# Kernel tuning notes

Hardware: AMD Instinct MI355X
Metric: run time of the kernel (lower is better)

## Reference

```python
import jax, jax.numpy as jnp
import numpy as np

EPS = 1e-3  # keras LayerNormalization default epsilon
H = 12     # number_of_heads


def _layer_norm(x, gamma, beta):
    mu = jnp.mean(x, axis=-1, keepdims=True)
    var = jnp.mean(jnp.square(x - mu), axis=-1, keepdims=True)
    return (x - mu) * jax.lax.rsqrt(var + EPS) * gamma + beta


def _gelu(x):
    return jax.nn.gelu(x, approximate=False)  # keras 'gelu' default is erf-based


def setup_inputs():
    key = jax.random.key(0)
    B, N, E, F, Fe = 8, 1024, 16384, 96, 32
    ks = jax.random.split(key, 20)
    def dense(k, din, dout):
        return jax.random.normal(k, (din, dout), jnp.float32) / np.float32(np.sqrt(din))
    return {
        "nodes": jax.random.normal(ks[0], (B, N, F), jnp.float32),
        "edge_features": jax.random.normal(ks[1], (B, E, Fe), jnp.float32),
        "edges": jax.random.randint(ks[2], (B, E, 2), 0, N),
        "edge_weights": jax.random.uniform(ks[3], (B, E, 1), jnp.float32),
        "edge_dropout": jnp.ones((B, E, 2), jnp.float32),
        # message layer: Dense(F) on concat([src,dst,edge_feat]) + GELU + LayerNorm
        "Wm": dense(ks[4], 2 * F + Fe, F), "bm": jnp.zeros((F,), jnp.float32),
        "gm": jnp.ones((F,), jnp.float32), "betam": jnp.zeros((F,), jnp.float32),
        # gated MHSA on concat([nodes, aggregated]) (2F -> F) + GELU + LayerNorm
        "Wq": dense(ks[5], 2 * F, F), "bq": jnp.zeros((F,), jnp.float32),
        "Wk": dense(ks[6], 2 * F, F), "bk": jnp.zeros((F,), jnp.float32),
        "Wv": dense(ks[7], 2 * F, F), "bv": jnp.zeros((F,), jnp.float32),
        "Wg": dense(ks[8], 2 * F, F), "bg": jnp.zeros((F,), jnp.float32),
        "Wo": dense(ks[9], F, F), "bo": jnp.zeros((F,), jnp.float32),
        "gu": jnp.ones((F,), jnp.float32), "betau": jnp.zeros((F,), jnp.float32),
    }


def reference(nodes, edge_features, edges, edge_weights, edge_dropout,
              Wm, bm, gm, betam, Wq, bq, Wk, bk, Wv, bv, Wg, bg, Wo, bo, gu, betau):
    B, N, F = nodes.shape
    E = edges.shape[1]
    # gather both endpoint features per edge: [B, E, 2F]
    gathered = jnp.take_along_axis(nodes, edges.reshape(B, 2 * E, 1), axis=1)
    msg_in = jnp.concatenate([gathered.reshape(B, E, 2 * F), edge_features], axis=-1)
    messages = _layer_norm(_gelu(msg_in @ Wm + bm), gm, betam)        # [B,E,F]
    weighted_messages = messages * edge_weights                        # [B,E,F]
    # batched scatter-sum onto target node edges[...,1], gated by dropout[...,1]
    contrib = weighted_messages * edge_dropout[..., 1:2]
    seg_ids = (edges[..., 1] + jnp.arange(B, dtype=edges.dtype)[:, None] * N).reshape(-1)
    aggregated = jax.ops.segment_sum(contrib.reshape(B * E, F), seg_ids,
                                     num_segments=B * N).reshape(B, N, F)
    # gated multi-head self-attention over concat(nodes, aggregated)
    x = jnp.concatenate([nodes, aggregated], axis=-1)                  # [B,N,2F]
    d = F // H
    def split_heads(y):
        return y.reshape(B, N, H, d).transpose(0, 2, 1, 3)             # [B,H,N,d]
    q = split_heads(x @ Wq + bq)
    k = split_heads(x @ Wk + bk)
    v = split_heads(x @ Wv + bv)
    gate = jax.nn.sigmoid(split_heads(x @ Wg + bg))
    scores = jnp.einsum("bhqd,bhkd->bhqk", q, k) / jnp.sqrt(jnp.float32(d))
    att = jnp.einsum("bhqk,bhkd->bhqd", jax.nn.softmax(scores, axis=-1), v) * gate
    att = att.transpose(0, 2, 1, 3).reshape(B, N, F)
    updated_nodes = _layer_norm(_gelu(att @ Wo + bo), gu, betau)
    return updated_nodes, weighted_messages, edges, edge_weights, edge_dropout
```

## Files before the change

kernel.cpp:

```cpp
#include <hip/hip_runtime.h>
#include <hip/hip_bf16.h>

#define BB 8
#define NN 1024
#define EE 16384
#define FF 96
#define FE 32
#define NH 12
#define DD 8
#define KM 224
#define KX 192
#define TE 64
#define BK 32

__device__ __forceinline__ float gelu_erf(float x){
    return 0.5f * x * (1.0f + erff(x * 0.70710678118654752f));
}

__device__ __forceinline__ int load_idx(const int* __restrict__ p, int i){
    int v = p[i];
    if (!((unsigned)v < 1024u)) v = (int)__int_as_float(v);
    return min(max(v, 0), NN-1);
}

__global__ __launch_bounds__(256) void hist_kernel(
    const int* __restrict__ edges, int* __restrict__ cnt)
{
    const int i = blockIdx.x*blockDim.x + threadIdx.x;
    if (i < BB*EE){
        const int b = i >> 14;
        const int dst = load_idx(edges, 2*i+1);
        atomicAdd(&cnt[b*NN + dst], 1);
    }
}

__global__ __launch_bounds__(1024) void scan_kernel(
    const int* __restrict__ cnt, int* __restrict__ rowstart, int* __restrict__ cursor)
{
    const int b = blockIdx.x;
    const int t = threadIdx.x;
    __shared__ int s[NN];
    const int v = cnt[b*NN + t];
    s[t] = v;
    __syncthreads();
    for (int off = 1; off < NN; off <<= 1){
        int u = (t >= off) ? s[t-off] : 0;
        __syncthreads();
        s[t] += u;
        __syncthreads();
    }
    const int ex = s[t] - v + b*EE;
    rowstart[b*NN + t] = ex;
    cursor[b*NN + t]   = ex;
}

__global__ __launch_bounds__(256) void scatter_kernel(
    const int* __restrict__ edges, int* __restrict__ cursor, int* __restrict__ elist)
{
    const int i = blockIdx.x*blockDim.x + threadIdx.x;
    if (i < BB*EE){
        const int b = i >> 14;
        const int dst = load_idx(edges, 2*i+1);
        const int pos = atomicAdd(&cursor[b*NN + dst], 1);
        elist[pos] = i;
    }
}

__global__ __launch_bounds__(256) void node_proj_kernel(
    const float* __restrict__ nodes, const float* __restrict__ Wm,
    float* __restrict__ P1, float* __restrict__ P2)
{
    const int rt  = blockIdx.x;
    const int m   = blockIdx.y;
    const int tid = threadIdx.x;
    const int tx  = tid & 15;
    const int ty  = tid >> 4;
    const int r0  = rt * TE;

    const float* W = Wm + (size_t)(m ? FF : 0) * FF;
    float* out     = m ? P2 : P1;

    __shared__ float Xs[TE][BK+4];
    __shared__ float Ws[BK][FF];

    float acc[4][6];
    #pragma unroll
    for (int a=0;a<4;++a)
        #pragma unroll
        for (int c=0;c<6;++c) acc[a][c] = 0.f;

    const int e_st = tid >> 2;
    const int kk0  = (tid & 3) * 8;

    for (int c = 0; c < 3; ++c){
        __syncthreads();
        {
            const float4* src = (const float4*)(W + (size_t)c*BK*FF);
            float4* dst = (float4*)&Ws[0][0];
            dst[tid      ] = src[tid      ];
            dst[tid + 256] = src[tid + 256];
            dst[tid + 512] = src[tid + 512];
        }
        {
            const float* rp = nodes + (size_t)(r0 + e_st)*FF + c*BK;
            *(float4*)&Xs[e_st][kk0    ] = *(const float4*)(rp + kk0);
            *(float4*)&Xs[e_st][kk0 + 4] = *(const float4*)(rp + kk0 + 4);
        }
        __syncthreads();
        #pragma unroll 4
        for (int kk = 0; kk < BK; ++kk){
            float2 w01 = *(const float2*)&Ws[kk][6*tx    ];
            float2 w23 = *(const float2*)&Ws[kk][6*tx + 2];
            float2 w45 = *(const float2*)&Ws[kk][6*tx + 4];
            float xv[4];
            #pragma unroll
            for (int ei=0; ei<4; ++ei) xv[ei] = Xs[ty + 16*ei][kk];
            #pragma unroll
            for (int ei=0; ei<4; ++ei){
                acc[ei][0] += xv[ei]*w01.x;  acc[ei][1] += xv[ei]*w01.y;
                acc[ei][2] += xv[ei]*w23.x;  acc[ei][3] += xv[ei]*w23.y;
                acc[ei][4] += xv[ei]*w45.x;  acc[ei][5] += xv[ei]*w45.y;
            }
        }
    }

    #pragma unroll
    for (int ei = 0; ei < 4; ++ei){
        const int row = r0 + ty + 16*ei;
        float* __restrict__ orow = out + (size_t)row*FF + 6*tx;
        #pragma unroll
        for (int jj=0; jj<6; ++jj) orow[jj] = acc[ei][jj];
    }
}

__global__ __launch_bounds__(256) void edge_msg2_kernel(
    const float* __restrict__ P1, const float* __restrict__ P2,
    const float* __restrict__ ef,
    const int*  __restrict__ edges, const float* __restrict__ ew,
    const float* __restrict__ Wm, const float* __restrict__ bm,
    const float* __restrict__ gm, const float* __restrict__ betam,
    float* __restrict__ wm_out)
{
    const int bid = blockIdx.x;
    const int tid = threadIdx.x;
    const int tx  = tid & 15;
    const int ty  = tid >> 4;
    const int be0 = bid * TE;
    const int b   = be0 >> 14;

    __shared__ float Xs[TE][BK+4];
    __shared__ float Ws[BK][FF];
    __shared__ int   eidx[TE*2];
    __shared__ float ewS[TE];
    __shared__ float bmS[FF], gmS[FF], betamS[FF];

    if (tid < TE*2){
        int v = edges[(size_t)be0*2 + tid];
        if (!((unsigned)v < 1024u)) v = (int)__int_as_float(v);
        eidx[tid] = min(max(v, 0), NN-1);
    }
    if (tid < TE) ewS[tid] = ew[be0 + tid];
    if (tid < FF){ bmS[tid] = bm[tid]; gmS[tid] = gm[tid]; betamS[tid] = betam[tid]; }

    float acc[4][6];
    #pragma unroll
    for (int a=0;a<4;++a)
        #pragma unroll
        for (int c=0;c<6;++c) acc[a][c] = 0.f;

    const int e_st = tid >> 2;
    const int kk0  = (tid & 3) * 8;

    {
        const float4* src = (const float4*)(Wm + (size_t)KX*FF);
        float4* dst = (float4*)&Ws[0][0];
        dst[tid      ] = src[tid      ];
        dst[tid + 256] = src[tid + 256];
        dst[tid + 512] = src[tid + 512];
    }
    {
        const float* rp = ef + (size_t)(be0 + e_st)*FE;
        *(float4*)&Xs[e_st][kk0    ] = *(const float4*)(rp + kk0);
        *(float4*)&Xs[e_st][kk0 + 4] = *(const float4*)(rp + kk0 + 4);
    }
    __syncthreads();
    #pragma unroll 4
    for (int kk = 0; kk < BK; ++kk){
        float2 w01 = *(const float2*)&Ws[kk][6*tx    ];
        float2 w23 = *(const float2*)&Ws[kk][6*tx + 2];
        float2 w45 = *(const float2*)&Ws[kk][6*tx + 4];
        float xv[4];
        #pragma unroll
        for (int ei=0; ei<4; ++ei) xv[ei] = Xs[ty + 16*ei][kk];
        #pragma unroll
        for (int ei=0; ei<4; ++ei){
            acc[ei][0] += xv[ei]*w01.x;  acc[ei][1] += xv[ei]*w01.y;
            acc[ei][2] += xv[ei]*w23.x;  acc[ei][3] += xv[ei]*w23.y;
            acc[ei][4] += xv[ei]*w45.x;  acc[ei][5] += xv[ei]*w45.y;
        }
    }

    float add[4][6];
    #pragma unroll
    for (int ei = 0; ei < 4; ++ei){
        const int el = ty + 16*ei;
        const int sn = eidx[2*el];
        const int dn = eidx[2*el+1];
        const float2* p1 = (const float2*)(P1 + (size_t)(b*NN + sn)*FF + 6*tx);
        const float2* p2 = (const float2*)(P2 + (size_t)(b*NN + dn)*FF + 6*tx);
        const float2 a0 = p1[0], a1 = p1[1], a2 = p1[2];
        const float2 b0 = p2[0], b1 = p2[1], b2 = p2[2];
        add[ei][0] = a0.x + b0.x;  add[ei][1] = a0.y + b0.y;
        add[ei][2] = a1.x + b1.x;  add[ei][3] = a1.y + b1.y;
        add[ei][4] = a2.x + b2.x;  add[ei][5] = a2.y + b2.y;
    }

    #pragma unroll
    for (int ei = 0; ei < 4; ++ei){
        const int el = ty + 16*ei;
        float h[6]; float psum = 0.f;
        #pragma unroll
        for (int jj=0; jj<6; ++jj){
            h[jj] = gelu_erf(acc[ei][jj] + add[ei][jj] + bmS[6*tx + jj]);
            psum += h[jj];
        }
        #pragma unroll
        for (int m=1; m<16; m<<=1) psum += __shfl_xor(psum, m, 16);
        const float mu = psum * (1.f/FF);
        float vsum = 0.f;
        #pragma unroll
        for (int jj=0; jj<6; ++jj){ float d = h[jj]-mu; vsum += d*d; }
        #pragma unroll
        for (int m=1; m<16; m<<=1) vsum += __shfl_xor(vsum, m, 16);
        const float rstd = rsqrtf(vsum*(1.f/FF) + 1e-3f);

        const float w = ewS[el];
        float* __restrict__ wrow = wm_out + (size_t)(be0 + el)*FF + 6*tx;
        #pragma unroll
        for (int jj=0; jj<6; ++jj)
            wrow[jj] = ((h[jj]-mu)*rstd*gmS[6*tx+jj] + betamS[6*tx+jj]) * w;
    }
}

__global__ __launch_bounds__(96) void gather_kernel(
    const float* __restrict__ wm_out, const float* __restrict__ ed,
    const int* __restrict__ elist, const int* __restrict__ rowstart,
    const int* __restrict__ cnt, float* __restrict__ agg)
{
    const int bn = blockIdx.x;
    const int t  = threadIdx.x;
    const int beg = rowstart[bn];
    const int num = cnt[bn];
    float sum = 0.f;
    for (int i = 0; i < num; ++i){
        const int be = elist[beg + i];
        const float coeff = ed[2*(size_t)be + 1];
        sum += wm_out[(size_t)be*FF + t] * coeff;
    }
    agg[(size_t)bn*FF + t] = sum;
}

__global__ __launch_bounds__(256) void qkvg_kernel(
    const float* __restrict__ nodes, const float* __restrict__ agg,
    const float* __restrict__ Wq, const float* __restrict__ bq,
    const float* __restrict__ Wk, const float* __restrict__ bk,
    const float* __restrict__ Wv, const float* __restrict__ bv,
    const float* __restrict__ Wg, const float* __restrict__ bg,
    float* __restrict__ qo, float* __restrict__ ko,
    float* __restrict__ vo, float* __restrict__ go)
{
    const int rt  = blockIdx.x;
    const int m   = blockIdx.y;
    const int tid = threadIdx.x;
    const int tx  = tid & 15;
    const int ty  = tid >> 4;
    const int r0  = rt * TE;

    const float* W    = (m==0)?Wq:(m==1)?Wk:(m==2)?Wv:Wg;
    const float* bias = (m==0)?bq:(m==1)?bk:(m==2)?bv:bg;
    float* out        = (m==0)?qo:(m==1)?ko:(m==2)?vo:go;

    __shared__ float Xs[TE][BK+4];
    __shared__ float Ws[BK][FF];
    __shared__ float bS[FF];
    if (tid < FF) bS[tid] = bias[tid];

    float acc[4][6];
    #pragma unroll
    for (int a=0;a<4;++a)
        #pragma unroll
        for (int c=0;c<6;++c) acc[a][c] = 0.f;

    const int e_st = tid >> 2;
    const int kk0  = (tid & 3) * 8;

    for (int c = 0; c < 6; ++c){
        __syncthreads();
        {
            const float4* src = (const float4*)(W + (size_t)c*BK*FF);
            float4* dst = (float4*)&Ws[0][0];
            dst[tid      ] = src[tid      ];
            dst[tid + 256] = src[tid + 256];
            dst[tid + 512] = src[tid + 512];
        }
        {
            const float* rp = (c < 3)
                ? nodes + (size_t)(r0 + e_st)*FF + c*BK
                : agg   + (size_t)(r0 + e_st)*FF + (c-3)*BK;
            *(float4*)&Xs[e_st][kk0    ] = *(const float4*)(rp + kk0);
            *(float4*)&Xs[e_st][kk0 + 4] = *(const float4*)(rp + kk0 + 4);
        }
        __syncthreads();
        #pragma unroll 4
        for (int kk = 0; kk < BK; ++kk){
            float2 w01 = *(const float2*)&Ws[kk][6*tx    ];
            float2 w23 = *(const float2*)&Ws[kk][6*tx + 2];
            float2 w45 = *(const float2*)&Ws[kk][6*tx + 4];
            float xv[4];
            #pragma unroll
            for (int ei=0; ei<4; ++ei) xv[ei] = Xs[ty + 16*ei][kk];
            #pragma unroll
            for (int ei=0; ei<4; ++ei){
                acc[ei][0] += xv[ei]*w01.x;  acc[ei][1] += xv[ei]*w01.y;
                acc[ei][2] += xv[ei]*w23.x;  acc[ei][3] += xv[ei]*w23.y;
                acc[ei][4] += xv[ei]*w45.x;  acc[ei][5] += xv[ei]*w45.y;
            }
        }
    }

    #pragma unroll
    for (int ei = 0; ei < 4; ++ei){
        const int row = r0 + ty + 16*ei;
        float* __restrict__ orow = out + (size_t)row*FF + 6*tx;
        #pragma unroll
        for (int jj=0; jj<6; ++jj) orow[jj] = acc[ei][jj] + bS[6*tx + jj];
    }
}

__global__ __launch_bounds__(256) void attn_kernel(
    const float* __restrict__ q, const float* __restrict__ k,
    const float* __restrict__ v, const float* g,
    float* att)
{
    const int blk = blockIdx.x;
    const int qt = blk & 15;
    const int h  = (blk >> 4) % NH;
    const int b  = blk / (16*NH);
    const int tid  = threadIdx.x;
    const int lane = tid & 63;
    const int w    = tid >> 6;
    const int r    = lane & 15;
    const int s    = lane >> 4;
    const int qrow = qt*64 + w*16 + r;
    const size_t base = (size_t)(b*NN)*FF + h*DD;

    __shared__ float Ks[128][12];
    __shared__ float Vs[128][12];

    float qr[DD];
    const float* qp = q + base + (size_t)qrow*FF;
    #pragma unroll
    for (int i=0;i<DD;++i) qr[i] = qp[i] * 0.35355339059327373f;

    float m = -1e30f, l = 0.f, o[DD];
    #pragma unroll
    for (int i=0;i<DD;++i) o[i] = 0.f;

    const int skey  = tid >> 1;
    const int shalf = (tid & 1) * 4;

    for (int kc = 0; kc < NN; kc += 128){
        __syncthreads();
        {
            const float* kp = k + base + (size_t)(kc + skey)*FF + shalf;
            const float* vp = v + base + (size_t)(kc + skey)*FF + shalf;
            *(float4*)&Ks[skey][shalf] = *(const float4*)kp;
            *(float4*)&Vs[skey][shalf] = *(const float4*)vp;
        }
        __syncthreads();
        #pragma unroll
        for (int gidx = 0; gidx < 4; ++gidx){
            float sc[8];
            #pragma unroll
            for (int jj = 0; jj < 8; ++jj){
                const int key = 32*gidx + 4*jj + s;
                float4 k0 = *(const float4*)&Ks[key][0];
                float4 k1 = *(const float4*)&Ks[key][4];
                sc[jj] = qr[0]*k0.x + qr[1]*k0.y + qr[2]*k0.z + qr[3]*k0.w
                       + qr[4]*k1.x + qr[5]*k1.y + qr[6]*k1.z + qr[7]*k1.w;
            }
            const float g01 = fmaxf(sc[0], sc[1]), g23 = fmaxf(sc[2], sc[3]);
            const float g45 = fmaxf(sc[4], sc[5]), g67 = fmaxf(sc[6], sc[7]);
            const float gmax = fmaxf(fmaxf(g01, g23), fmaxf(g45, g67));
            if (gmax > m + 8.f){
                const float c = __expf(m - gmax);
                l *= c;
                #pragma unroll
                for (int i=0;i<DD;++i) o[i] *= c;
                m = gmax;
            }
            #pragma unroll
            for (int jj = 0; jj < 8; ++jj){
                const int key = 32*gidx + 4*jj + s;
                float4 v0 = *(const float4*)&Vs[key][0];
                float4 v1 = *(const float4*)&Vs[key][4];
                const float p = __expf(sc[jj] - m);
                l += p;
                o[0] += p*v0.x;  o[1] += p*v0.y;
                o[2] += p*v0.z;  o[3] += p*v0.w;
                o[4] += p*v1.x;  o[5] += p*v1.y;
                o[6] += p*v1.z;  o[7] += p*v1.w;
            }
        }
    }

    #pragma unroll
    for (int mask = 16; mask <= 32; mask <<= 1){
        const float m2 = __shfl_xor(m, mask);
        const float l2 = __shfl_xor(l, mask);
        float o2[DD];
        #pragma unroll
        for (int i=0;i<DD;++i) o2[i] = __shfl_xor(o[i], mask);
        const float M  = fmaxf(m, m2);
        const float c1 = __expf(m - M);
        const float c2 = __expf(m2 - M);
        l = l*c1 + l2*c2;
        #pragma unroll
        for (int i=0;i<DD;++i) o[i] = o[i]*c1 + o2[i]*c2;
        m = M;
    }

    if (s == 0){
        const float inv = 1.f / l;
        const float* gp = g + base + (size_t)qrow*FF;
        float* ap = att + base + (size_t)qrow*FF;
        #pragma unroll
        for (int i=0;i<DD;++i){
            const float gate = 1.f/(1.f + __expf(-gp[i]));
            ap[i] = o[i]*inv*gate;
        }
    }
}

__global__ __launch_bounds__(256) void out_kernel(
    const float* __restrict__ att, const float* __restrict__ Wo, const float* __restrict__ bo,
    const float* __restrict__ gu, const float* __restrict__ betau,
    float* __restrict__ out0)
{
    const int rt  = blockIdx.x;
    const int tid = threadIdx.x;
    const int tx  = tid & 15;
    const int ty  = tid >> 4;
    const int r0  = rt * TE;

    __shared__ float Xs[TE][BK+4];
    __shared__ float Ws[BK][FF];
    __shared__ float boS[FF], guS[FF], beS[FF];
    if (tid < FF){ boS[tid] = bo[tid]; guS[tid] = gu[tid]; beS[tid] = betau[tid]; }

    float acc[4][6];
    #pragma unroll
    for (int a=0;a<4;++a)
        #pragma unroll
        for (int c=0;c<6;++c) acc[a][c] = 0.f;

    const int e_st = tid >> 2;
    const int kk0  = (tid & 3) * 8;

    for (int c = 0; c < 3; ++c){
        __syncthreads();
        {
            const float4* src = (const float4*)(Wo + (size_t)c*BK*FF);
            float4* dst = (float4*)&Ws[0][0];
            dst[tid      ] = src[tid      ];
            dst[tid + 256] = src[tid + 256];
            dst[tid + 512] = src[tid + 512];
        }
        {
            const float* rp = att + (size_t)(r0 + e_st)*FF + c*BK;
            *(float4*)&Xs[e_st][kk0    ] = *(const float4*)(rp + kk0);
            *(float4*)&Xs[e_st][kk0 + 4] = *(const float4*)(rp + kk0 + 4);
        }
        __syncthreads();
        #pragma unroll 4
        for (int kk = 0; kk < BK; ++kk){
            float2 w01 = *(const float2*)&Ws[kk][6*tx    ];
            float2 w23 = *(const float2*)&Ws[kk][6*tx + 2];
            float2 w45 = *(const float2*)&Ws[kk][6*tx + 4];
            float xv[4];
            #pragma unroll
            for (int ei=0; ei<4; ++ei) xv[ei] = Xs[ty + 16*ei][kk];
            #pragma unroll
            for (int ei=0; ei<4; ++ei){
                acc[ei][0] += xv[ei]*w01.x;  acc[ei][1] += xv[ei]*w01.y;
                acc[ei][2] += xv[ei]*w23.x;  acc[ei][3] += xv[ei]*w23.y;
                acc[ei][4] += xv[ei]*w45.x;  acc[ei][5] += xv[ei]*w45.y;
            }
        }
    }

    #pragma unroll
    for (int ei = 0; ei < 4; ++ei){
        const int row = r0 + ty + 16*ei;
        float h[6]; float psum = 0.f;
        #pragma unroll
        for (int jj=0; jj<6; ++jj){
            h[jj] = gelu_erf(acc[ei][jj] + boS[6*tx + jj]);
            psum += h[jj];
        }
        #pragma unroll
        for (int m=1; m<16; m<<=1) psum += __shfl_xor(psum, m, 16);
        const float mu = psum * (1.f/FF);
        float vsum = 0.f;
        #pragma unroll
        for (int jj=0; jj<6; ++jj){ float d = h[jj]-mu; vsum += d*d; }
        #pragma unroll
        for (int m=1; m<16; m<<=1) vsum += __shfl_xor(vsum, m, 16);
        const float rstd = rsqrtf(vsum*(1.f/FF) + 1e-3f);
        float* __restrict__ orow = out0 + (size_t)row*FF + 6*tx;
        #pragma unroll
        for (int jj=0; jj<6; ++jj)
            orow[jj] = (h[jj]-mu)*rstd*guS[6*tx+jj] + beS[6*tx+jj];
    }
}

__global__ void passthrough_kernel(const int* __restrict__ edges,
    const float* __restrict__ ew, const float* __restrict__ ed,
    float* __restrict__ o_edges, float* __restrict__ o_ew, float* __restrict__ o_ed)
{
    const int i = blockIdx.x*blockDim.x + threadIdx.x;
    const int NE2 = BB*EE*2;
    const int NW  = BB*EE;
    if (i < NE2)                 o_edges[i] = (float)load_idx(edges, i);
    else if (i < NE2+NW)         o_ew[i-NE2] = ew[i-NE2];
    else if (i < NE2+NW+NE2)     o_ed[i-NE2-NW] = ed[i-NE2-NW];
}

extern "C" void kernel_launch(void* const* d_in, const int* in_sizes, int n_in,
                              void* d_out, int out_size, void* d_ws, size_t ws_size,
                              hipStream_t stream) {
    int i_nodes=-1, i_ef=-1, i_edges=-1, i_ed=-1, i_ew=-1, i_Wm=-1, i_Wo=-1;
    int i_W4[4]; int nW4=0;
    int i_v96[10]; int nv96=0;
    for (int i = 0; i < n_in; ++i){
        const int s = in_sizes[i];
        if      (s == 786432)  i_nodes = i;
        else if (s == 4194304) i_ef = i;
        else if (s == 262144)  { if (i_edges < 0) i_edges = i; else i_ed = i; }
        else if (s == 131072)  i_ew = i;
        else if (s == 21504)   i_Wm = i;
        else if (s == 18432)   { if (nW4 < 4) i_W4[nW4++] = i; }
        else if (s == 9216)    i_Wo = i;
        else if (s == 96)      { if (nv96 < 10) i_v96[nv96++] = i; }
    }
    const float* nodes = (const float*)d_in[i_nodes];
    const float* ef    = (const float*)d_in[i_ef];
    const int*   edges = (const int*)d_in[i_edges];
    const float* ew    = (const float*)d_in[i_ew];
    const float* ed    = (const float*)d_in[i_ed];
    const float* Wm = (const float*)d_in[i_Wm];
    const float* Wq = (const float*)d_in[i_W4[0]];
    const float* Wk = (const float*)d_in[i_W4[1]];
    const float* Wv = (const float*)d_in[i_W4[2]];
    const float* Wg = (const float*)d_in[i_W4[3]];
    const float* Wo = (const float*)d_in[i_Wo];
    const float* bm    = (const float*)d_in[i_v96[0]];
    const float* gm    = (const float*)d_in[i_v96[1]];
    const float* betam = (const float*)d_in[i_v96[2]];
    const float* bq    = (const float*)d_in[i_v96[3]];
    const float* bk    = (const float*)d_in[i_v96[4]];
    const float* bv    = (const float*)d_in[i_v96[5]];
    const float* bg    = (const float*)d_in[i_v96[6]];
    const float* bo    = (const float*)d_in[i_v96[7]];
    const float* gu    = (const float*)d_in[i_v96[8]];
    const float* betau = (const float*)d_in[i_v96[9]];

    float* outp = (float*)d_out;
    const size_t ROWS  = (size_t)BB*NN*FF;
    const size_t WMSZ  = (size_t)BB*EE*FF;
    const size_t NE2   = (size_t)BB*EE*2;
    const size_t NW    = (size_t)BB*EE;
    float* out_un    = outp;
    float* out_wm    = outp + ROWS;
    float* out_edges = outp + ROWS + WMSZ;
    float* out_ew    = outp + ROWS + WMSZ + NE2;
    float* out_ed    = outp + ROWS + WMSZ + NE2 + NW;

    float* ws  = (float*)d_ws;
    float* agg = ws;
    float* qo  = ws + 1*ROWS;
    float* ko  = ws + 2*ROWS;
    float* vo  = ws + 3*ROWS;
    float* go  = ws + 4*ROWS;
    float* att = go;
    float* P1  = qo;
    float* P2  = ko;
    int* ints      = (int*)(ws + 5*ROWS);
    int* cnt       = ints;
    int* rowstart  = ints + BB*NN;
    int* cursor    = ints + 2*BB*NN;
    int* elist     = ints + 3*BB*NN;

    hipMemsetAsync(cnt, 0, BB*NN*sizeof(int), stream);

    hist_kernel<<<(BB*EE+255)/256, 256, 0, stream>>>(edges, cnt);
    scan_kernel<<<BB, NN, 0, stream>>>(cnt, rowstart, cursor);
    scatter_kernel<<<(BB*EE+255)/256, 256, 0, stream>>>(edges, cursor, elist);

    dim3 npgrid((BB*NN)/TE, 2);
    node_proj_kernel<<<npgrid, 256, 0, stream>>>(nodes, Wm, P1, P2);

    edge_msg2_kernel<<<(BB*EE)/TE, 256, 0, stream>>>(P1, P2, ef, edges, ew,
                                               Wm, bm, gm, betam, out_wm);
    gather_kernel<<<BB*NN, 96, 0, stream>>>(out_wm, ed, elist, rowstart, cnt, agg);

    dim3 qgrid((BB*NN)/TE, 4);
    qkvg_kernel<<<qgrid, 256, 0, stream>>>(nodes, agg, Wq, bq, Wk, bk, Wv, bv,
                                           Wg, bg, qo, ko, vo, go);
    attn_kernel<<<BB*NH*16, 256, 0, stream>>>(qo, ko, vo, go, att);
    out_kernel<<<(BB*NN)/TE, 256, 0, stream>>>(att, Wo, bo, gu, betau, out_un);

    const int npass = (int)(NE2 + NW + NE2);
    passthrough_kernel<<<(npass+255)/256, 256, 0, stream>>>(edges, ew, ed,
                                               out_edges, out_ew, out_ed);
}
```

Before: 311.6 us.

## Register-block attention over four query rows per thread to reuse shared K/V loads

```diff
diff --git a/kernel.cpp b/kernel.cpp
--- a/kernel.cpp
+++ b/kernel.cpp
@@ -337,7 +337,7 @@
     }
 }
 
-__global__ __launch_bounds__(256) void attn_kernel(
+__global__ __launch_bounds__(256, 4) void attn_kernel(
     const float* __restrict__ q, const float* __restrict__ k,
     const float* __restrict__ v, const float* g,
     float* att)
@@ -349,22 +349,29 @@
     const int tid  = threadIdx.x;
     const int lane = tid & 63;
     const int w    = tid >> 6;
-    const int r    = lane & 15;
-    const int s    = lane >> 4;
-    const int qrow = qt*64 + w*16 + r;
+    const int rg   = lane >> 4;
+    const int s    = lane & 15;
+    const int row0 = qt*64 + w*16 + rg*4;
     const size_t base = (size_t)(b*NN)*FF + h*DD;
 
     __shared__ float Ks[128][12];
     __shared__ float Vs[128][12];
 
-    float qr[DD];
-    const float* qp = q + base + (size_t)qrow*FF;
-    #pragma unroll
-    for (int i=0;i<DD;++i) qr[i] = qp[i] * 0.35355339059327373f;
-
-    float m = -1e30f, l = 0.f, o[DD];
-    #pragma unroll
-    for (int i=0;i<DD;++i) o[i] = 0.f;
+    float qr[4][DD];
+    #pragma unroll
+    for (int i=0;i<4;++i){
+        const float* qp = q + base + (size_t)(row0+i)*FF;
+        #pragma unroll
+        for (int d0=0; d0<DD; ++d0) qr[i][d0] = qp[d0] * 0.35355339059327373f;
+    }
+
+    float m[4], l[4], o[4][DD];
+    #pragma unroll
+    for (int i=0;i<4;++i){
+        m[i] = -1e30f; l[i] = 0.f;
+        #pragma unroll
+        for (int d0=0; d0<DD; ++d0) o[i][d0] = 0.f;
+    }
 
     const int skey  = tid >> 1;
     const int shalf = (tid & 1) * 4;
@@ -379,65 +386,80 @@
         }
         __syncthreads();
         #pragma unroll
-        for (int gidx = 0; gidx < 4; ++gidx){
-            float sc[8];
-            #pragma unroll
-            for (int jj = 0; jj < 8; ++jj){
-                const int key = 32*gidx + 4*jj + s;
-                float4 k0 = *(const float4*)&Ks[key][0];
-                float4 k1 = *(const float4*)&Ks[key][4];
-                sc[jj] = qr[0]*k0.x + qr[1]*k0.y + qr[2]*k0.z + qr[3]*k0.w
-                       + qr[4]*k1.x + qr[5]*k1.y + qr[6]*k1.z + qr[7]*k1.w;
+        for (int g2 = 0; g2 < 2; ++g2){
+            float sc[4][4];
+            #pragma unroll
+            for (int j=0;j<4;++j){
+                const int key = g2*64 + j*16 + s;
+                const float4 k0 = *(const float4*)&Ks[key][0];
+                const float4 k1 = *(const float4*)&Ks[key][4];
+                #pragma unroll
+                for (int i=0;i<4;++i){
+                    sc[i][j] = qr[i][0]*k0.x + qr[i][1]*k0.y + qr[i][2]*k0.z + qr[i][3]*k0.w
+                             + qr[i][4]*k1.x + qr[i][5]*k1.y + qr[i][6]*k1.z + qr[i][7]*k1.w;
+                }
             }
-            const float g01 = fmaxf(sc[0], sc[1]), g23 = fmaxf(sc[2], sc[3]);
-            const float g45 = fmaxf(sc[4], sc[5]), g67 = fmaxf(sc[6], sc[7]);
-            const float gmax = fmaxf(fmaxf(g01, g23), fmaxf(g45, g67));
-            if (gmax > m + 8.f){
-                const float c = __expf(m - gmax);
-                l *= c;
+            #pragma unroll
+            for (int i=0;i<4;++i){
+                const float gmax = fmaxf(fmaxf(sc[i][0], sc[i][1]),
+                                         fmaxf(sc[i][2], sc[i][3]));
+                if (gmax > m[i] + 8.f){
+                    const float c = __expf(m[i] - gmax);
+                    l[i] *= c;
+                    #pragma unroll
+                    for (int d0=0; d0<DD; ++d0) o[i][d0] *= c;
+                    m[i] = gmax;
+                }
+            }
+            #pragma unroll
+            for (int j=0;j<4;++j){
+                const int key = g2*64 + j*16 + s;
+                const float4 v0 = *(const float4*)&Vs[key][0];
+                const float4 v1 = *(const float4*)&Vs[key][4];
                 #pragma unroll
-                for (int i=0;i<DD;++i) o[i] *= c;
-                m = gmax;
+                for (int i=0;i<4;++i){
+                    const float p = __expf(sc[i][j] - m[i]);
+                    l[i] += p;
+                    o[i][0] += p*v0.x;  o[i][1] += p*v0.y;
+                    o[i][2] += p*v0.z;  o[i][3] += p*v0.w;
+                    o[i][4] += p*v1.x;  o[i][5] += p*v1.y;
+                    o[i][6] += p*v1.z;  o[i][7] += p*v1.w;
+                }
             }
-            #pragma unroll
-            for (int jj = 0; jj < 8; ++jj){
-                const int key = 32*gidx + 4*jj + s;
-                float4 v0 = *(const float4*)&Vs[key][0];
-                float4 v1 = *(const float4*)&Vs[key][4];
-                const float p = __expf(sc[jj] - m);
-                l += p;
-                o[0] += p*v0.x;  o[1] += p*v0.y;
-                o[2] += p*v0.z;  o[3] += p*v0.w;
-                o[4] += p*v1.x;  o[5] += p*v1.y;
-                o[6] += p*v1.z;  o[7] += p*v1.w;
+        }
+    }
+
+    #pragma unroll
+    for (int mask = 1; mask <= 8; mask <<= 1){
+        #pragma unroll
+        for (int i=0;i<4;++i){
+            const float m2 = __shfl_xor(m[i], mask);
+            const float l2 = __shfl_xor(l[i], mask);
+            float o2[DD];
+            #pragma unroll
+            for (int d0=0; d0<DD; ++d0) o2[d0] = __shfl_xor(o[i][d0], mask);
+            const float M  = fmaxf(m[i], m2);
+            const float c1 = __expf(m[i] - M);
+            const float c2 = __expf(m2 - M);
+            l[i] = l[i]*c1 + l2*c2;
+            #pragma unroll
+            for (int d0=0; d0<DD; ++d0) o[i][d0] = o[i][d0]*c1 + o2[d0]*c2;
+            m[i] = M;
+        }
+    }
+
+    if (s == 0){
+        #pragma unroll
+        for (int i=0;i<4;++i){
+            const int row = row0 + i;
+            const float inv = 1.f / l[i];
+            const float* gp = g + base + (size_t)row*FF;
+            float* ap = att + base + (size_t)row*FF;
+            #pragma unroll
+            for (int d0=0; d0<DD; ++d0){
+                const float gate = 1.f/(1.f + __expf(-gp[d0]));
+                ap[d0] = o[i][d0]*inv*gate;
             }
-        }
-    }
-
-    #pragma unroll
-    for (int mask = 16; mask <= 32; mask <<= 1){
-        const float m2 = __shfl_xor(m, mask);
-        const float l2 = __shfl_xor(l, mask);
-        float o2[DD];
-        #pragma unroll
-        for (int i=0;i<DD;++i) o2[i] = __shfl_xor(o[i], mask);
-        const float M  = fmaxf(m, m2);
-        const float c1 = __expf(m - M);
-        const float c2 = __expf(m2 - M);
-        l = l*c1 + l2*c2;
-        #pragma unroll
-        for (int i=0;i<DD;++i) o[i] = o[i]*c1 + o2[i]*c2;
-        m = M;
-    }
-
-    if (s == 0){
-        const float inv = 1.f / l;
-        const float* gp = g + base + (size_t)qrow*FF;
-        float* ap = att + base + (size_t)qrow*FF;
-        #pragma unroll
-        for (int i=0;i<DD;++i){
-            const float gate = 1.f/(1.f + __expf(-gp[i]));
-            ap[i] = o[i]*inv*gate;
         }
     }
 }
```

New measurement: 511.9 us. +64.3%, slower.

## Double-buffer K/V tiles in attention and switch softmax to exp2 domain

Applied to the files above, without the earlier changes.

```diff
diff --git a/kernel.cpp b/kernel.cpp
--- a/kernel.cpp
+++ b/kernel.cpp
@@ -13,6 +13,12 @@
 #define TE 64
 #define BK 32
 
+#if __has_builtin(__builtin_amdgcn_exp2f)
+#define EXP2(x) __builtin_amdgcn_exp2f(x)
+#else
+#define EXP2(x) exp2f(x)
+#endif
+
 __device__ __forceinline__ float gelu_erf(float x){
     return 0.5f * x * (1.0f + erff(x * 0.70710678118654752f));
 }
@@ -354,13 +360,13 @@
     const int qrow = qt*64 + w*16 + r;
     const size_t base = (size_t)(b*NN)*FF + h*DD;
 
-    __shared__ float Ks[128][12];
-    __shared__ float Vs[128][12];
+    __shared__ float Ks[2][128][12];
+    __shared__ float Vs[2][128][12];
 
     float qr[DD];
     const float* qp = q + base + (size_t)qrow*FF;
     #pragma unroll
-    for (int i=0;i<DD;++i) qr[i] = qp[i] * 0.35355339059327373f;
+    for (int i=0;i<DD;++i) qr[i] = qp[i] * 0.51010300101462254f;
 
     float m = -1e30f, l = 0.f, o[DD];
     #pragma unroll
@@ -369,31 +375,37 @@
     const int skey  = tid >> 1;
     const int shalf = (tid & 1) * 4;
 
-    for (int kc = 0; kc < NN; kc += 128){
-        __syncthreads();
-        {
-            const float* kp = k + base + (size_t)(kc + skey)*FF + shalf;
-            const float* vp = v + base + (size_t)(kc + skey)*FF + shalf;
-            *(float4*)&Ks[skey][shalf] = *(const float4*)kp;
-            *(float4*)&Vs[skey][shalf] = *(const float4*)vp;
-        }
-        __syncthreads();
+    float4 kreg, vreg;
+    {
+        const float* kp = k + base + (size_t)skey*FF + shalf;
+        const float* vp = v + base + (size_t)skey*FF + shalf;
+        kreg = *(const float4*)kp;
+        vreg = *(const float4*)vp;
+        *(float4*)&Ks[0][skey][shalf] = kreg;
+        *(float4*)&Vs[0][skey][shalf] = vreg;
+        kreg = *(const float4*)(k + base + (size_t)(128 + skey)*FF + shalf);
+        vreg = *(const float4*)(v + base + (size_t)(128 + skey)*FF + shalf);
+    }
+    __syncthreads();
+
+    for (int t = 0; t < 8; ++t){
+        const int buf = t & 1;
         #pragma unroll
         for (int gidx = 0; gidx < 4; ++gidx){
             float sc[8];
             #pragma unroll
             for (int jj = 0; jj < 8; ++jj){
                 const int key = 32*gidx + 4*jj + s;
-                float4 k0 = *(const float4*)&Ks[key][0];
-                float4 k1 = *(const float4*)&Ks[key][4];
+                float4 k0 = *(const float4*)&Ks[buf][key][0];
+                float4 k1 = *(const float4*)&Ks[buf][key][4];
                 sc[jj] = qr[0]*k0.x + qr[1]*k0.y + qr[2]*k0.z + qr[3]*k0.w
                        + qr[4]*k1.x + qr[5]*k1.y + qr[6]*k1.z + qr[7]*k1.w;
             }
             const float g01 = fmaxf(sc[0], sc[1]), g23 = fmaxf(sc[2], sc[3]);
             const float g45 = fmaxf(sc[4], sc[5]), g67 = fmaxf(sc[6], sc[7]);
             const float gmax = fmaxf(fmaxf(g01, g23), fmaxf(g45, g67));
-            if (gmax > m + 8.f){
-                const float c = __expf(m - gmax);
+            if (gmax > m + 11.5f){
+                const float c = EXP2(m - gmax);
                 l *= c;
                 #pragma unroll
                 for (int i=0;i<DD;++i) o[i] *= c;
@@ -402,9 +414,9 @@
             #pragma unroll
             for (int jj = 0; jj < 8; ++jj){
                 const int key = 32*gidx + 4*jj + s;
-                float4 v0 = *(const float4*)&Vs[key][0];
-                float4 v1 = *(const float4*)&Vs[key][4];
-                const float p = __expf(sc[jj] - m);
+                float4 v0 = *(const float4*)&Vs[buf][key][0];
+                float4 v1 = *(const float4*)&Vs[buf][key][4];
+                const float p = EXP2(sc[jj] - m);
                 l += p;
                 o[0] += p*v0.x;  o[1] += p*v0.y;
                 o[2] += p*v0.z;  o[3] += p*v0.w;
@@ -412,6 +424,15 @@
                 o[6] += p*v1.z;  o[7] += p*v1.w;
             }
         }
+        if (t < 7){
+            *(float4*)&Ks[buf^1][skey][shalf] = kreg;
+            *(float4*)&Vs[buf^1][skey][shalf] = vreg;
+            __syncthreads();
+            if (t < 6){
+                kreg = *(const float4*)(k + base + (size_t)((t+2)*128 + skey)*FF + shalf);
+                vreg = *(const float4*)(v + base + (size_t)((t+2)*128 + skey)*FF + shalf);
+            }
+        }
     }
 
     #pragma unroll
@@ -422,8 +443,8 @@
         #pragma unroll
         for (int i=0;i<DD;++i) o2[i] = __shfl_xor(o[i], mask);
         const float M  = fmaxf(m, m2);
-        const float c1 = __expf(m - M);
-        const float c2 = __expf(m2 - M);
+        const float c1 = EXP2(m - M);
+        const float c2 = EXP2(m2 - M);
         l = l*c1 + l2*c2;
         #pragma unroll
         for (int i=0;i<DD;++i) o[i] = o[i]*c1 + o2[i]*c2;
```

Result: no change. 312.6 us (+0.3%).
